# Kernel optimization log

Hardware: AMD Instinct MI355X
Metric: run time of the kernel (lower is better)

Reference implementation:

```python
import jax, jax.numpy as jnp
import numpy as np


def setup_inputs() -> dict:
    key = jax.random.key(0)
    kq, kk, kv = jax.random.split(key, 3)
    B, H, N, D = 4, 16, 2048, 64
    q = jax.random.normal(kq, (B, H, N, D), dtype=jnp.float32)
    k = jax.random.normal(kk, (B, N, D), dtype=jnp.float32)
    v = jax.random.normal(kv, (B, N, D), dtype=jnp.float32)
    return {"q": q, "k": k, "v": v}


def reference(q, k, v):
    # q: [B,H,N,D], k/v: [B,N,D] (KV shared across heads)
    scale = q.shape[-1] ** -0.5
    sim = jnp.einsum('bhid,bjd->bhij', q, k) * scale  # [B,H,N,N]
    attn = jax.nn.softmax(sim, axis=-1)
    return jnp.einsum('bhij,bjd->bhid', attn, v)  # [B,H,N,D]
```

## Files before the change

### kernel.cpp

```cpp
#include <hip/hip_runtime.h>
#include <hip/hip_bf16.h>

#define B_ 4
#define H_ 16
#define N_ 2048
#define D_ 64
#define BM 128
#define BN 64

typedef __bf16 bf16;
typedef bf16 bf16x4 __attribute__((ext_vector_type(4)));
typedef bf16 bf16x8 __attribute__((ext_vector_type(8)));
typedef float f32x4 __attribute__((ext_vector_type(4)));

#define SCALE_LOG2E 0.18033688011112042f

#define GBL(p) ((const __attribute__((address_space(1))) void*)(p))
#define LDS(p) ((__attribute__((address_space(3))) void*)(p))

__global__ __launch_bounds__(256) void convert_kv(const float* __restrict__ k,
                                                  const float* __restrict__ v,
                                                  bf16* __restrict__ kbf_sw,
                                                  bf16* __restrict__ vtf_sw) {
    const int tile = blockIdx.x >> 1;
    const int rep  = blockIdx.x & 1;
    const int b = tile >> 5, T = tile & 31;
    const int t = threadIdx.x;

    const int p  = t + rep * 256;
    const int r  = p >> 3;
    const int up = p & 7;
    const int u  = up ^ (r & 7);
    {
        const float* src = k + ((size_t)(b * N_ + T * 64 + r) * D_ + u * 8);
        float4 a = *(const float4*)src;
        float4 c = *(const float4*)(src + 4);
        bf16x8 o;
        o[0] = (bf16)a.x; o[1] = (bf16)a.y; o[2] = (bf16)a.z; o[3] = (bf16)a.w;
        o[4] = (bf16)c.x; o[5] = (bf16)c.y; o[6] = (bf16)c.z; o[7] = (bf16)c.w;
        *(bf16x8*)(kbf_sw + (size_t)tile * 4096 + p * 8) = o;
    }
    {
        const float* src = v + ((size_t)(b * N_ + T * 64 + u * 8) * D_ + r);
        bf16x8 o;
        #pragma unroll
        for (int j = 0; j < 8; ++j) o[j] = (bf16)src[(size_t)j * D_];
        *(bf16x8*)(vtf_sw + (size_t)tile * 4096 + p * 8) = o;
    }
}

__global__ __launch_bounds__(256, 4) void attn_fwd(const float* __restrict__ q,
                                                   const bf16* __restrict__ kbf_sw,
                                                   const bf16* __restrict__ vtf_sw,
                                                   float* __restrict__ out) {
    __shared__ __align__(16) bf16 KV[2][2][4096];
    __shared__ __align__(16) bf16 Ps[4][1024];

    const int tid  = threadIdx.x;
    const int lane = tid & 63;
    const int wv   = tid >> 6;
    const int quad = lane >> 4;
    const int n16  = lane & 15;
    const int h7   = n16 & 7;

    const int bh = blockIdx.y;
    const int b  = bh >> 4;
    const int q0 = blockIdx.x * BM + wv * 32;

    const bf16* ktiles = kbf_sw + (size_t)b * 32 * 4096;
    const bf16* vtiles = vtf_sw + (size_t)b * 32 * 4096;

    bf16x8 qf[2][2];
    #pragma unroll
    for (int qt = 0; qt < 2; ++qt)
        #pragma unroll
        for (int ks = 0; ks < 2; ++ks) {
            const float* src = q + ((size_t)bh * N_ + q0 + qt * 16 + n16) * D_ + ks * 32 + quad * 8;
            float4 a = *(const float4*)src;
            float4 c = *(const float4*)(src + 4);
            bf16x8 pk;
            pk[0] = (bf16)(a.x * SCALE_LOG2E); pk[1] = (bf16)(a.y * SCALE_LOG2E);
            pk[2] = (bf16)(a.z * SCALE_LOG2E); pk[3] = (bf16)(a.w * SCALE_LOG2E);
            pk[4] = (bf16)(c.x * SCALE_LOG2E); pk[5] = (bf16)(c.y * SCALE_LOG2E);
            pk[6] = (bf16)(c.z * SCALE_LOG2E); pk[7] = (bf16)(c.w * SCALE_LOG2E);
            qf[qt][ks] = pk;
        }

    f32x4 acc[4][2];
    #pragma unroll
    for (int dt = 0; dt < 4; ++dt)
        #pragma unroll
        for (int qt = 0; qt < 2; ++qt) {
            acc[dt][qt][0] = 0.f; acc[dt][qt][1] = 0.f;
            acc[dt][qt][2] = 0.f; acc[dt][qt][3] = 0.f;
        }
    float lacc[2] = {0.f, 0.f};

    auto issue_dma = [&](int it, int p) {
        #pragma unroll
        for (int j = 0; j < 2; ++j) {
            const int c = wv * 2 + j;
            __builtin_amdgcn_global_load_lds(
                GBL(ktiles + (size_t)it * 4096 + c * 512 + lane * 8),
                LDS(&KV[p][0][c * 512]), 16, 0, 0);
            __builtin_amdgcn_global_load_lds(
                GBL(vtiles + (size_t)it * 4096 + c * 512 + lane * 8),
                LDS(&KV[p][1][c * 512]), 16, 0, 0);
        }
    };

    issue_dma(0, 0);
    bf16* Pw = &Ps[wv][0];

    for (int it = 0; it < N_ / BN; ++it) {
        const int p = it & 1;
        __syncthreads();
        if (it + 1 < N_ / BN) issue_dma(it + 1, p ^ 1);

        bf16x8 kf[4][2], vf[2][4];
        #pragma unroll
        for (int kt = 0; kt < 4; ++kt)
            #pragma unroll
            for (int ks = 0; ks < 2; ++ks)
                kf[kt][ks] = *(const bf16x8*)&KV[p][0][(kt * 16 + n16) * 64 + ((4 * ks + quad) ^ h7) * 8];
        #pragma unroll
        for (int ks = 0; ks < 2; ++ks)
            #pragma unroll
            for (int dt = 0; dt < 4; ++dt)
                vf[ks][dt] = *(const bf16x8*)&KV[p][1][(dt * 16 + n16) * 64 + ((4 * ks + quad) ^ h7) * 8];

        #pragma unroll
        for (int qt = 0; qt < 2; ++qt) {
            f32x4 s[4];
            #pragma unroll
            for (int kt = 0; kt < 4; ++kt) {
                s[kt][0] = 0.f; s[kt][1] = 0.f; s[kt][2] = 0.f; s[kt][3] = 0.f;
            }
            #pragma unroll
            for (int kt = 0; kt < 4; ++kt) {
                s[kt] = __builtin_amdgcn_mfma_f32_16x16x32_bf16(kf[kt][0], qf[qt][0], s[kt], 0, 0, 0);
                s[kt] = __builtin_amdgcn_mfma_f32_16x16x32_bf16(kf[kt][1], qf[qt][1], s[kt], 0, 0, 0);
            }
            #pragma unroll
            for (int kt = 0; kt < 4; ++kt) {
                f32x4 pv;
                #pragma unroll
                for (int r = 0; r < 4; ++r) pv[r] = __builtin_amdgcn_exp2f(s[kt][r]);
                lacc[qt] += (pv[0] + pv[1]) + (pv[2] + pv[3]);
                bf16x4 pb;
                pb[0] = (bf16)pv[0]; pb[1] = (bf16)pv[1];
                pb[2] = (bf16)pv[2]; pb[3] = (bf16)pv[3];
                const int u = 2 * kt + (quad >> 1);
                *(bf16x4*)&Pw[n16 * 64 + ((u ^ h7) * 8) + (quad & 1) * 4] = pb;
            }
            #pragma unroll
            for (int ks = 0; ks < 2; ++ks) {
                bf16x8 pb = *(const bf16x8*)&Pw[n16 * 64 + ((4 * ks + quad) ^ h7) * 8];
                #pragma unroll
                for (int dt = 0; dt < 4; ++dt)
                    acc[dt][qt] = __builtin_amdgcn_mfma_f32_16x16x32_bf16(vf[ks][dt], pb, acc[dt][qt], 0, 0, 0);
            }
        }
    }

    #pragma unroll
    for (int qt = 0; qt < 2; ++qt) {
        float l = lacc[qt];
        l += __shfl_xor(l, 16);
        l += __shfl_xor(l, 32);
        float inv = 1.0f / l;
        const int qrow = q0 + qt * 16 + n16;
        float* dst = out + (size_t)(bh * N_ + qrow) * D_ + quad * 4;
        #pragma unroll
        for (int dt = 0; dt < 4; ++dt) {
            float4 o;
            o.x = acc[dt][qt][0] * inv; o.y = acc[dt][qt][1] * inv;
            o.z = acc[dt][qt][2] * inv; o.w = acc[dt][qt][3] * inv;
            *(float4*)(dst + dt * 16) = o;
        }
    }
}

extern "C" void kernel_launch(void* const* d_in, const int* in_sizes, int n_in,
                              void* d_out, int out_size, void* d_ws, size_t ws_size,
                              hipStream_t stream) {
    const float* q = (const float*)d_in[0];
    const float* k = (const float*)d_in[1];
    const float* v = (const float*)d_in[2];
    float* out = (float*)d_out;

    bf16* kbf_sw = (bf16*)d_ws;
    bf16* vtf_sw = kbf_sw + (size_t)B_ * N_ * D_;

    convert_kv<<<B_ * 64, 256, 0, stream>>>(k, v, kbf_sw, vtf_sw);
    dim3 grid(N_ / BM, B_ * H_);
    attn_fwd<<<grid, 256, 0, stream>>>(q, kbf_sw, vtf_sw, out);
}
```

Before: 164.5 us.

## Switch attention to 32x32x16 MFMA with register-shuffled P fragments

```diff
diff --git a/kernel.cpp b/kernel.cpp
--- a/kernel.cpp
+++ b/kernel.cpp
@@ -5,13 +5,14 @@
 #define H_ 16
 #define N_ 2048
 #define D_ 64
-#define BM 128
+#define BM 256
 #define BN 64
 
 typedef __bf16 bf16;
 typedef bf16 bf16x4 __attribute__((ext_vector_type(4)));
 typedef bf16 bf16x8 __attribute__((ext_vector_type(8)));
-typedef float f32x4 __attribute__((ext_vector_type(4)));
+typedef float f32x2 __attribute__((ext_vector_type(2)));
+typedef float f32x16 __attribute__((ext_vector_type(16)));
 
 #define SCALE_LOG2E 0.18033688011112042f
 
@@ -20,62 +21,71 @@
 
 __global__ __launch_bounds__(256) void convert_kv(const float* __restrict__ k,
                                                   const float* __restrict__ v,
-                                                  bf16* __restrict__ kbf_sw,
-                                                  bf16* __restrict__ vtf_sw) {
+                                                  bf16* __restrict__ img) {
     const int tile = blockIdx.x >> 1;
-    const int rep  = blockIdx.x & 1;
     const int b = tile >> 5, T = tile & 31;
-    const int t = threadIdx.x;
+    const int pu = (blockIdx.x & 1) * 256 + threadIdx.x;
+    const int mtks = pu >> 6;
+    const int ln   = pu & 63;
+    const int mt = mtks >> 2, ks = mtks & 3;
+    bf16* timg = img + (size_t)tile * 8192;
 
-    const int p  = t + rep * 256;
-    const int r  = p >> 3;
-    const int up = p & 7;
-    const int u  = up ^ (r & 7);
     {
-        const float* src = k + ((size_t)(b * N_ + T * 64 + r) * D_ + u * 8);
+        const int kvr = T * 64 + mt * 32 + (ln & 31);
+        const int d0  = ks * 16 + (ln >> 5) * 8;
+        const float* src = k + ((size_t)b * N_ + kvr) * D_ + d0;
         float4 a = *(const float4*)src;
         float4 c = *(const float4*)(src + 4);
         bf16x8 o;
         o[0] = (bf16)a.x; o[1] = (bf16)a.y; o[2] = (bf16)a.z; o[3] = (bf16)a.w;
         o[4] = (bf16)c.x; o[5] = (bf16)c.y; o[6] = (bf16)c.z; o[7] = (bf16)c.w;
-        *(bf16x8*)(kbf_sw + (size_t)tile * 4096 + p * 8) = o;
+        *(bf16x8*)(timg + pu * 8) = o;
     }
     {
-        const float* src = v + ((size_t)(b * N_ + T * 64 + u * 8) * D_ + r);
+        const int d   = mt * 32 + (ln & 31);
+        const int kv0 = T * 64 + ks * 16 + (ln >> 5) * 8;
+        const float* src = v + ((size_t)b * N_ + kv0) * D_ + d;
         bf16x8 o;
         #pragma unroll
         for (int j = 0; j < 8; ++j) o[j] = (bf16)src[(size_t)j * D_];
-        *(bf16x8*)(vtf_sw + (size_t)tile * 4096 + p * 8) = o;
+        *(bf16x8*)(timg + 4096 + pu * 8) = o;
     }
 }
 
-__global__ __launch_bounds__(256, 4) void attn_fwd(const float* __restrict__ q,
-                                                   const bf16* __restrict__ kbf_sw,
-                                                   const bf16* __restrict__ vtf_sw,
+static __device__ inline bf16x4 pack4(float a, float b, float c, float d) {
+    bf16x4 r; r[0] = (bf16)a; r[1] = (bf16)b; r[2] = (bf16)c; r[3] = (bf16)d; return r;
+}
+static __device__ inline bf16x4 xor32(bf16x4 x) {
+    f32x2 f = __builtin_bit_cast(f32x2, x);
+    f32x2 g;
+    g[0] = __shfl_xor(f[0], 32);
+    g[1] = __shfl_xor(f[1], 32);
+    return __builtin_bit_cast(bf16x4, g);
+}
+
+__global__ __launch_bounds__(256, 2) void attn_fwd(const float* __restrict__ q,
+                                                   const bf16* __restrict__ img,
                                                    float* __restrict__ out) {
-    __shared__ __align__(16) bf16 KV[2][2][4096];
-    __shared__ __align__(16) bf16 Ps[4][1024];
+    __shared__ __align__(16) bf16 KV[2][8192];
 
     const int tid  = threadIdx.x;
     const int lane = tid & 63;
     const int wv   = tid >> 6;
-    const int quad = lane >> 4;
-    const int n16  = lane & 15;
-    const int h7   = n16 & 7;
+    const int half = lane >> 5;
+    const int l31  = lane & 31;
 
     const int bh = blockIdx.y;
     const int b  = bh >> 4;
-    const int q0 = blockIdx.x * BM + wv * 32;
+    const int q0 = blockIdx.x * BM + wv * 64;
 
-    const bf16* ktiles = kbf_sw + (size_t)b * 32 * 4096;
-    const bf16* vtiles = vtf_sw + (size_t)b * 32 * 4096;
+    const bf16* tiles = img + (size_t)b * 32 * 8192;
 
-    bf16x8 qf[2][2];
+    bf16x8 qf[2][4];
     #pragma unroll
-    for (int qt = 0; qt < 2; ++qt)
+    for (int qn = 0; qn < 2; ++qn)
         #pragma unroll
-        for (int ks = 0; ks < 2; ++ks) {
-            const float* src = q + ((size_t)bh * N_ + q0 + qt * 16 + n16) * D_ + ks * 32 + quad * 8;
+        for (int ks = 0; ks < 4; ++ks) {
+            const float* src = q + ((size_t)bh * N_ + q0 + qn * 32 + l31) * D_ + ks * 16 + half * 8;
             float4 a = *(const float4*)src;
             float4 c = *(const float4*)(src + 4);
             bf16x8 pk;
@@ -83,101 +93,88 @@
             pk[2] = (bf16)(a.z * SCALE_LOG2E); pk[3] = (bf16)(a.w * SCALE_LOG2E);
             pk[4] = (bf16)(c.x * SCALE_LOG2E); pk[5] = (bf16)(c.y * SCALE_LOG2E);
             pk[6] = (bf16)(c.z * SCALE_LOG2E); pk[7] = (bf16)(c.w * SCALE_LOG2E);
-            qf[qt][ks] = pk;
+            qf[qn][ks] = pk;
         }
 
-    f32x4 acc[4][2];
-    #pragma unroll
-    for (int dt = 0; dt < 4; ++dt)
-        #pragma unroll
-        for (int qt = 0; qt < 2; ++qt) {
-            acc[dt][qt][0] = 0.f; acc[dt][qt][1] = 0.f;
-            acc[dt][qt][2] = 0.f; acc[dt][qt][3] = 0.f;
-        }
+    f32x16 acc[2][2] = {{{}, {}}, {{}, {}}};
     float lacc[2] = {0.f, 0.f};
 
     auto issue_dma = [&](int it, int p) {
+        const bf16* g = tiles + (size_t)it * 8192;
         #pragma unroll
-        for (int j = 0; j < 2; ++j) {
-            const int c = wv * 2 + j;
-            __builtin_amdgcn_global_load_lds(
-                GBL(ktiles + (size_t)it * 4096 + c * 512 + lane * 8),
-                LDS(&KV[p][0][c * 512]), 16, 0, 0);
-            __builtin_amdgcn_global_load_lds(
-                GBL(vtiles + (size_t)it * 4096 + c * 512 + lane * 8),
-                LDS(&KV[p][1][c * 512]), 16, 0, 0);
+        for (int j = 0; j < 4; ++j) {
+            const int c = wv * 4 + j;
+            __builtin_amdgcn_global_load_lds(GBL(g + c * 512 + lane * 8),
+                                             LDS(&KV[p][c * 512]), 16, 0, 0);
         }
     };
 
     issue_dma(0, 0);
-    bf16* Pw = &Ps[wv][0];
 
     for (int it = 0; it < N_ / BN; ++it) {
         const int p = it & 1;
         __syncthreads();
         if (it + 1 < N_ / BN) issue_dma(it + 1, p ^ 1);
 
-        bf16x8 kf[4][2], vf[2][4];
+        bf16x8 kf[2][4], vf[2][4];
         #pragma unroll
-        for (int kt = 0; kt < 4; ++kt)
+        for (int mt = 0; mt < 2; ++mt)
             #pragma unroll
-            for (int ks = 0; ks < 2; ++ks)
-                kf[kt][ks] = *(const bf16x8*)&KV[p][0][(kt * 16 + n16) * 64 + ((4 * ks + quad) ^ h7) * 8];
-        #pragma unroll
-        for (int ks = 0; ks < 2; ++ks)
-            #pragma unroll
-            for (int dt = 0; dt < 4; ++dt)
-                vf[ks][dt] = *(const bf16x8*)&KV[p][1][(dt * 16 + n16) * 64 + ((4 * ks + quad) ^ h7) * 8];
+            for (int ks = 0; ks < 4; ++ks) {
+                kf[mt][ks] = *(const bf16x8*)&KV[p][((mt * 4 + ks) * 64 + lane) * 8];
+                vf[mt][ks] = *(const bf16x8*)&KV[p][4096 + ((mt * 4 + ks) * 64 + lane) * 8];
+            }
 
         #pragma unroll
-        for (int qt = 0; qt < 2; ++qt) {
-            f32x4 s[4];
+        for (int qn = 0; qn < 2; ++qn) {
+            f32x16 s[2] = {{}, {}};
             #pragma unroll
-            for (int kt = 0; kt < 4; ++kt) {
-                s[kt][0] = 0.f; s[kt][1] = 0.f; s[kt][2] = 0.f; s[kt][3] = 0.f;
+            for (int ks = 0; ks < 4; ++ks) {
+                s[0] = __builtin_amdgcn_mfma_f32_32x32x16_bf16(kf[0][ks], qf[qn][ks], s[0], 0, 0, 0);
+                s[1] = __builtin_amdgcn_mfma_f32_32x32x16_bf16(kf[1][ks], qf[qn][ks], s[1], 0, 0, 0);
             }
             #pragma unroll
-            for (int kt = 0; kt < 4; ++kt) {
-                s[kt] = __builtin_amdgcn_mfma_f32_16x16x32_bf16(kf[kt][0], qf[qt][0], s[kt], 0, 0, 0);
-                s[kt] = __builtin_amdgcn_mfma_f32_16x16x32_bf16(kf[kt][1], qf[qt][1], s[kt], 0, 0, 0);
-            }
-            #pragma unroll
-            for (int kt = 0; kt < 4; ++kt) {
-                f32x4 pv;
+            for (int mt = 0; mt < 2; ++mt) {
+                float pv[16];
                 #pragma unroll
-                for (int r = 0; r < 4; ++r) pv[r] = __builtin_amdgcn_exp2f(s[kt][r]);
-                lacc[qt] += (pv[0] + pv[1]) + (pv[2] + pv[3]);
-                bf16x4 pb;
-                pb[0] = (bf16)pv[0]; pb[1] = (bf16)pv[1];
-                pb[2] = (bf16)pv[2]; pb[3] = (bf16)pv[3];
-                const int u = 2 * kt + (quad >> 1);
-                *(bf16x4*)&Pw[n16 * 64 + ((u ^ h7) * 8) + (quad & 1) * 4] = pb;
-            }
-            #pragma unroll
-            for (int ks = 0; ks < 2; ++ks) {
-                bf16x8 pb = *(const bf16x8*)&Pw[n16 * 64 + ((4 * ks + quad) ^ h7) * 8];
+                for (int r = 0; r < 16; ++r) pv[r] = __builtin_amdgcn_exp2f(s[mt][r]);
+                float t0 = 0.f, t1 = 0.f;
                 #pragma unroll
-                for (int dt = 0; dt < 4; ++dt)
-                    acc[dt][qt] = __builtin_amdgcn_mfma_f32_16x16x32_bf16(vf[ks][dt], pb, acc[dt][qt], 0, 0, 0);
+                for (int r = 0; r < 8; ++r) { t0 += pv[r]; t1 += pv[8 + r]; }
+                lacc[qn] += t0 + t1;
+                #pragma unroll
+                for (int sp = 0; sp < 2; ++sp) {
+                    bf16x4 lo  = pack4(pv[8 * sp + 0], pv[8 * sp + 1], pv[8 * sp + 2], pv[8 * sp + 3]);
+                    bf16x4 hi  = pack4(pv[8 * sp + 4], pv[8 * sp + 5], pv[8 * sp + 6], pv[8 * sp + 7]);
+                    bf16x4 xlo = xor32(lo), xhi = xor32(hi);
+                    bf16x4 a0 = half ? xhi : lo;
+                    bf16x4 a1 = half ? hi  : xlo;
+                    bf16x8 bfrag = __builtin_shufflevector(a0, a1, 0, 1, 2, 3, 4, 5, 6, 7);
+                    const int g = mt * 2 + sp;
+                    acc[0][qn] = __builtin_amdgcn_mfma_f32_32x32x16_bf16(vf[0][g], bfrag, acc[0][qn], 0, 0, 0);
+                    acc[1][qn] = __builtin_amdgcn_mfma_f32_32x32x16_bf16(vf[1][g], bfrag, acc[1][qn], 0, 0, 0);
+                }
             }
         }
     }
 
     #pragma unroll
-    for (int qt = 0; qt < 2; ++qt) {
-        float l = lacc[qt];
-        l += __shfl_xor(l, 16);
-        l += __shfl_xor(l, 32);
+    for (int qn = 0; qn < 2; ++qn) {
+        float l = lacc[qn] + __shfl_xor(lacc[qn], 32);
         float inv = 1.0f / l;
-        const int qrow = q0 + qt * 16 + n16;
-        float* dst = out + (size_t)(bh * N_ + qrow) * D_ + quad * 4;
+        const int qrow = q0 + qn * 32 + l31;
+        float* dst = out + ((size_t)bh * N_ + qrow) * D_ + 4 * half;
         #pragma unroll
-        for (int dt = 0; dt < 4; ++dt) {
-            float4 o;
-            o.x = acc[dt][qt][0] * inv; o.y = acc[dt][qt][1] * inv;
-            o.z = acc[dt][qt][2] * inv; o.w = acc[dt][qt][3] * inv;
-            *(float4*)(dst + dt * 16) = o;
-        }
+        for (int mt = 0; mt < 2; ++mt)
+            #pragma unroll
+            for (int rq = 0; rq < 4; ++rq) {
+                float4 o;
+                o.x = acc[mt][qn][4 * rq + 0] * inv;
+                o.y = acc[mt][qn][4 * rq + 1] * inv;
+                o.z = acc[mt][qn][4 * rq + 2] * inv;
+                o.w = acc[mt][qn][4 * rq + 3] * inv;
+                *(float4*)(dst + mt * 32 + 8 * rq) = o;
+            }
     }
 }
 
@@ -189,10 +186,9 @@
     const float* v = (const float*)d_in[2];
     float* out = (float*)d_out;
 
-    bf16* kbf_sw = (bf16*)d_ws;
-    bf16* vtf_sw = kbf_sw + (size_t)B_ * N_ * D_;
+    bf16* img = (bf16*)d_ws;
 
-    convert_kv<<<B_ * 64, 256, 0, stream>>>(k, v, kbf_sw, vtf_sw);
+    convert_kv<<<B_ * 64, 256, 0, stream>>>(k, v, img);
     dim3 grid(N_ / BM, B_ * H_);
-    attn_fwd<<<grid, 256, 0, stream>>>(q, kbf_sw, vtf_sw, out);
+    attn_fwd<<<grid, 256, 0, stream>>>(q, img, out);
 }
```

New measurement: 155.3 us. 5.6% less time.
